# Performance work log

Measured on AMD Instinct MI355X. Metric: run time of the kernel, lower is better.

The kernel has to match this reference:

```python
import jax, jax.numpy as jnp
import numpy as np

B, T, C = 2, 2048, 1024
N_HEAD = 16
D_HEAD = C // N_HEAD


def setup_inputs() -> dict:
    key = jax.random.key(0)
    ks = jax.random.split(key, 5)
    x = jax.random.normal(ks[0], (B, T, C), dtype=jnp.float32)
    W_attn = jax.random.normal(ks[1], (C, 3 * C), dtype=jnp.float32) * (1.0 / np.sqrt(C))
    b_attn = jax.random.normal(ks[2], (3 * C,), dtype=jnp.float32) * 0.02
    W_proj = jax.random.normal(ks[3], (C, C), dtype=jnp.float32) * (1.0 / np.sqrt(C))
    b_proj = jax.random.normal(ks[4], (C,), dtype=jnp.float32) * 0.02
    return {"x": x, "W_attn": W_attn, "b_attn": b_attn, "W_proj": W_proj, "b_proj": b_proj}


def reference(x, W_attn, b_attn, W_proj, b_proj):
    b, t, c = x.shape
    nh, dh = N_HEAD, c // N_HEAD
    # qkv projection: (B, T, 3C) -> (B, T, 3, nh, dh) -> (B, nh, 3, T, dh)
    a = (x @ W_attn + b_attn).reshape(b, t, 3, nh, dh).transpose(0, 3, 2, 1, 4)
    Q, K, V = a[:, :, 0], a[:, :, 1], a[:, :, 2]  # each (B, nh, T, dh)
    # naive full attention: no causal mask, no pre-softmax scaling (as in source)
    scores = jnp.einsum('bhqd,bhkd->bhqk', Q, K)  # (B, nh, T, T) -- 512 MB
    att = jax.nn.softmax(scores, axis=-1)
    y = jnp.einsum('bhqk,bhkd->bhqd', att, V) / jnp.sqrt(jnp.asarray(dh, x.dtype))
    y = y.transpose(0, 2, 1, 3).reshape(b, t, c)  # (B, T, C)
    return y @ W_proj + b_proj
```

## Files before the change

### kernel.cpp

```cpp
#include <hip/hip_runtime.h>

typedef _Float16 f16;
typedef f16  f16x8 __attribute__((ext_vector_type(8)));
typedef f16  f16x4 __attribute__((ext_vector_type(4)));
typedef float f32x4 __attribute__((ext_vector_type(4)));
typedef int  i32x4 __attribute__((ext_vector_type(4)));

#define MFMA16(a,b,c) __builtin_amdgcn_mfma_f32_16x16x32_f16((a),(b),(c),0,0,0)
#define EXP2(x) __builtin_amdgcn_exp2f(x)
#define LOG2E 1.44269504089f

static constexpr int Tq   = 2048;
static constexpr int Cdim = 1024;

__device__ static inline void gload_lds16(const f16* gsrc, f16* ldst)
{
    __builtin_amdgcn_global_load_lds(
        (const __attribute__((address_space(1))) void*)gsrc,
        (__attribute__((address_space(3))) void*)ldst, 16, 0, 0);
}

__global__ __launch_bounds__(256) void k_cvt_x(const float* __restrict__ x, f16* __restrict__ xh)
{
    int i = blockIdx.x * 256 + threadIdx.x;
    f32x4 v = ((const f32x4*)x)[i];
    f16x4 o; o[0] = (f16)v[0]; o[1] = (f16)v[1]; o[2] = (f16)v[2]; o[3] = (f16)v[3];
    ((f16x4*)xh)[i] = o;
}

__global__ __launch_bounds__(256) void k_trans(const float* __restrict__ W, f16* __restrict__ WT,
                                               int K, int N)
{
    __shared__ float t[64][65];
    int n0 = blockIdx.x * 64, k0 = blockIdx.y * 64;
    int tid = threadIdx.x;
    int lr = tid >> 6, lc = tid & 63;
    #pragma unroll 4
    for (int i = 0; i < 16; i++) {
        int kl = lr * 16 + i;
        t[kl][lc] = W[(size_t)(k0 + kl) * N + n0 + lc];
    }
    __syncthreads();
    #pragma unroll 4
    for (int i = 0; i < 16; i++) {
        int nl = lr * 16 + i;
        WT[(size_t)(n0 + nl) * K + k0 + lc] = (f16)t[lc][nl];
    }
}

template<int EPI>
__global__ __launch_bounds__(256) void k_gemm(
    const f16* __restrict__ A, const f16* __restrict__ BT, const float* __restrict__ bias,
    float* __restrict__ Cf, f16* __restrict__ Qc, f16* __restrict__ Kc, f16* __restrict__ Vt,
    int N, int K)
{
    __shared__ __align__(16) f16 As[128][64];
    __shared__ __align__(16) f16 Bs[128][64];
    const int tid = threadIdx.x;
    const int lane = tid & 63, wv = tid >> 6;
    const int l16 = lane & 15, lhi = lane >> 4;
    const int wr = wv >> 1, wc = wv & 1;
    const int bm = blockIdx.y * 128, bn = blockIdx.x * 128;

    const int srow = lane >> 3;
    const int sch  = (lane & 7) ^ (srow & 7);

    f32x4 acc[4][4] = {};

    for (int kt = 0; kt < K; kt += 64) {
        #pragma unroll
        for (int i = 0; i < 4; i++) {
            int blk = wv * 4 + i;
            int row = blk * 8 + srow;
            gload_lds16(A  + (size_t)(bm + row) * K + kt + sch * 8, &As[blk * 8][0]);
            gload_lds16(BT + (size_t)(bn + row) * K + kt + sch * 8, &Bs[blk * 8][0]);
        }
        __syncthreads();
        #pragma unroll
        for (int kk = 0; kk < 2; kk++) {
            f16x8 af[4], bfr[4];
            #pragma unroll
            for (int i = 0; i < 4; i++) {
                int ra = wr * 64 + i * 16 + l16;
                af[i]  = *(const f16x8*)&As[ra][((kk * 4 + lhi) ^ (ra & 7)) * 8];
                int rb = wc * 64 + i * 16 + l16;
                bfr[i] = *(const f16x8*)&Bs[rb][((kk * 4 + lhi) ^ (rb & 7)) * 8];
            }
            #pragma unroll
            for (int i = 0; i < 4; i++)
                #pragma unroll
                for (int j = 0; j < 4; j++)
                    acc[i][j] = MFMA16(af[i], bfr[j], acc[i][j]);
        }
        __syncthreads();
    }

    #pragma unroll
    for (int i = 0; i < 4; i++) {
        int row0 = bm + wr * 64 + i * 16 + lhi * 4;
        #pragma unroll
        for (int j = 0; j < 4; j++) {
            int col = bn + wc * 64 + j * 16 + l16;
            float bv = bias[col];
            if (EPI == 0) {
                #pragma unroll
                for (int r = 0; r < 4; r++)
                    Cf[(size_t)(row0 + r) * N + col] = acc[i][j][r] + bv;
            } else {
                int b_ = row0 >> 11;
                int t0 = row0 & 2047;
                int s  = col >> 10;
                int h  = (col >> 6) & 15;
                int d  = col & 63;
                int bh = b_ * 16 + h;
                if (s < 2) {
                    f16* dst = (s == 0 ? Qc : Kc);
                    #pragma unroll
                    for (int r = 0; r < 4; r++)
                        dst[((size_t)bh * Tq + t0 + r) * 64 + d] = (f16)(acc[i][j][r] + bv);
                } else {
                    f16x4 p;
                    #pragma unroll
                    for (int r = 0; r < 4; r++) p[r] = (f16)(acc[i][j][r] + bv);
                    *(f16x4*)&Vt[((size_t)bh * 64 + d) * Tq + t0] = p;
                }
            }
        }
    }
}

__global__ __launch_bounds__(256) void k_attn(
    const f16* __restrict__ Qc, const f16* __restrict__ Kc, const f16* __restrict__ Vt,
    f16* __restrict__ Yc)
{
    __shared__ __align__(16) f16 Ks[2][64][64];
    __shared__ __align__(16) f16 Vs[2][64][64];

    const int tid = threadIdx.x;
    const int lane = tid & 63, wv = tid >> 6;
    const int l16 = lane & 15, lhi = lane >> 4;
    const int bh = blockIdx.y;
    const int q0 = blockIdx.x * 64;

    const f16* Qh = Qc + (size_t)bh * Tq * 64;
    const f16* Kh = Kc + (size_t)bh * Tq * 64;
    const f16* Vh = Vt + (size_t)bh * 64 * Tq;

    const int row0 = tid >> 3, ch0 = tid & 7;
    const int rp0  = (((row0 >> 2) & 1) << 4) | (((row0 >> 4) & 1) << 3)
                   | (((row0 >> 3) & 1) << 2) | (row0 & 3);
    const int pchK = ch0 ^ (rp0 & 7);
    const int pchV = ch0 ^ (row0 & 7);

    f16x8 qf[2];
    {
        int qrow = q0 + wv * 16 + l16;
        #pragma unroll
        for (int kk = 0; kk < 2; kk++)
            qf[kk] = *(const f16x8*)(Qh + (size_t)qrow * 64 + kk * 32 + lhi * 8);
    }

    f32x4 o[4] = {};
    float m2 = -3e38f, l = 0.0f;

    f16x8 kr0, kr1, vr0, vr1;
    kr0 = *(const f16x8*)(Kh + (size_t)row0 * 64 + ch0 * 8);
    kr1 = *(const f16x8*)(Kh + (size_t)(row0 + 32) * 64 + ch0 * 8);
    vr0 = *(const f16x8*)(Vh + (size_t)row0 * Tq + ch0 * 8);
    vr1 = *(const f16x8*)(Vh + (size_t)(row0 + 32) * Tq + ch0 * 8);
    *(f16x8*)&Ks[0][rp0][pchK * 8]       = kr0;
    *(f16x8*)&Ks[0][rp0 + 32][pchK * 8]  = kr1;
    *(f16x8*)&Vs[0][row0][pchV * 8]      = vr0;
    *(f16x8*)&Vs[0][row0 + 32][pchV * 8] = vr1;
    __syncthreads();

    int cur = 0;
    for (int t = 0; t < 32; t++) {
        if (t < 31) {
            int kt2 = (t + 1) * 64;
            kr0 = *(const f16x8*)(Kh + (size_t)(kt2 + row0) * 64 + ch0 * 8);
            kr1 = *(const f16x8*)(Kh + (size_t)(kt2 + row0 + 32) * 64 + ch0 * 8);
            vr0 = *(const f16x8*)(Vh + (size_t)row0 * Tq + kt2 + ch0 * 8);
            vr1 = *(const f16x8*)(Vh + (size_t)(row0 + 32) * Tq + kt2 + ch0 * 8);
        }

        const f16 (* __restrict__ Kb)[64] = Ks[cur];
        const f16 (* __restrict__ Vb)[64] = Vs[cur];

        f32x4 s[4];
        __builtin_amdgcn_s_setprio(1);
        #pragma unroll
        for (int ck = 0; ck < 4; ck++) {
            f32x4 acc = {};
            #pragma unroll
            for (int kk = 0; kk < 2; kk++) {
                f16x8 kf = *(const f16x8*)&Kb[ck * 16 + l16][((kk * 4 + lhi) ^ (l16 & 7)) * 8];
                acc = MFMA16(kf, qf[kk], acc);
            }
            s[ck] = acc;
        }
        __builtin_amdgcn_s_setprio(0);

        float tm = fmaxf(
            fmaxf(fmaxf(fmaxf(s[0][0], s[0][1]), fmaxf(s[0][2], s[0][3])),
                  fmaxf(fmaxf(s[1][0], s[1][1]), fmaxf(s[1][2], s[1][3]))),
            fmaxf(fmaxf(fmaxf(s[2][0], s[2][1]), fmaxf(s[2][2], s[2][3])),
                  fmaxf(fmaxf(s[3][0], s[3][1]), fmaxf(s[3][2], s[3][3]))));
        tm = fmaxf(tm, __shfl_xor(tm, 16));
        tm = fmaxf(tm, __shfl_xor(tm, 32));

        if (!__all(tm - m2 <= 8.0f)) {
            float mn = fmaxf(m2, tm);
            float sc = EXP2((m2 - mn) * LOG2E);
            m2 = mn; l *= sc;
            #pragma unroll
            for (int ct = 0; ct < 4; ct++)
                #pragma unroll
                for (int r = 0; r < 4; r++)
                    o[ct][r] *= sc;
        }

        float nm2 = -m2 * LOG2E;
        f32x4 p[4];
        #pragma unroll
        for (int ck = 0; ck < 4; ck++)
            #pragma unroll
            for (int r = 0; r < 4; r++)
                p[ck][r] = EXP2(fmaf(s[ck][r], LOG2E, nm2));

        float su = ((p[0][0] + p[0][1]) + (p[0][2] + p[0][3]))
                 + ((p[1][0] + p[1][1]) + (p[1][2] + p[1][3]))
                 + ((p[2][0] + p[2][1]) + (p[2][2] + p[2][3]))
                 + ((p[3][0] + p[3][1]) + (p[3][2] + p[3][3]));
        su += __shfl_xor(su, 16);
        su += __shfl_xor(su, 32);
        l += su;

        __builtin_amdgcn_s_setprio(1);
        #pragma unroll
        for (int kk2 = 0; kk2 < 2; kk2++) {
            i32x4 w;
            w[0] = __builtin_bit_cast(int, __builtin_amdgcn_cvt_pkrtz(p[2*kk2][0],   p[2*kk2][1]));
            w[1] = __builtin_bit_cast(int, __builtin_amdgcn_cvt_pkrtz(p[2*kk2][2],   p[2*kk2][3]));
            w[2] = __builtin_bit_cast(int, __builtin_amdgcn_cvt_pkrtz(p[2*kk2+1][0], p[2*kk2+1][1]));
            w[3] = __builtin_bit_cast(int, __builtin_amdgcn_cvt_pkrtz(p[2*kk2+1][2], p[2*kk2+1][3]));
            f16x8 pb = __builtin_bit_cast(f16x8, w);
            #pragma unroll
            for (int ct = 0; ct < 4; ct++) {
                f16x8 vf = *(const f16x8*)&Vb[ct * 16 + l16][((kk2 * 4 + lhi) ^ (l16 & 7)) * 8];
                o[ct] = MFMA16(vf, pb, o[ct]);
            }
        }
        __builtin_amdgcn_s_setprio(0);

        if (t < 31) {
            int nxt = cur ^ 1;
            *(f16x8*)&Ks[nxt][rp0][pchK * 8]       = kr0;
            *(f16x8*)&Ks[nxt][rp0 + 32][pchK * 8]  = kr1;
            *(f16x8*)&Vs[nxt][row0][pchV * 8]      = vr0;
            *(f16x8*)&Vs[nxt][row0 + 32][pchV * 8] = vr1;
            __syncthreads();
            cur = nxt;
        }
    }

    const int b_ = bh >> 4, h_ = bh & 15;
    const int q  = q0 + wv * 16 + l16;
    const float inv = 1.0f / (l * 8.0f);
    size_t rb = (size_t)(b_ * Tq + q) * Cdim + h_ * 64;
    #pragma unroll
    for (int ct = 0; ct < 4; ct++) {
        f16x4 y;
        #pragma unroll
        for (int r = 0; r < 4; r++) y[r] = (f16)(o[ct][r] * inv);
        *(f16x4*)&Yc[rb + ct * 16 + lhi * 4] = y;
    }
}

extern "C" void kernel_launch(void* const* d_in, const int* in_sizes, int n_in,
                              void* d_out, int out_size, void* d_ws, size_t ws_size,
                              hipStream_t stream)
{
    (void)in_sizes; (void)n_in; (void)out_size; (void)ws_size;
    const float* x  = (const float*)d_in[0];
    const float* Wa = (const float*)d_in[1];
    const float* ba = (const float*)d_in[2];
    const float* Wp = (const float*)d_in[3];
    const float* bp = (const float*)d_in[4];
    float* out = (float*)d_out;

    char* ws = (char*)d_ws;
    f16* Xh  = (f16*)(ws);
    f16* WaT = (f16*)(ws + (8u  << 20));
    f16* WpT = (f16*)(ws + (14u << 20));
    f16* Qc  = (f16*)(ws + (16u << 20));
    f16* Kc  = (f16*)(ws + (24u << 20));
    f16* Vt  = (f16*)(ws + (32u << 20));
    f16* Yc  = (f16*)(ws + (40u << 20));

    k_cvt_x<<<4096, 256, 0, stream>>>(x, Xh);
    k_trans<<<dim3(48, 16), 256, 0, stream>>>(Wa, WaT, 1024, 3072);
    k_trans<<<dim3(16, 16), 256, 0, stream>>>(Wp, WpT, 1024, 1024);
    k_gemm<1><<<dim3(24, 32), 256, 0, stream>>>(Xh, WaT, ba, nullptr, Qc, Kc, Vt, 3072, 1024);
    k_attn<<<dim3(32, 32), 256, 0, stream>>>(Qc, Kc, Vt, Yc);
    k_gemm<0><<<dim3(8, 32), 256, 0, stream>>>(Yc, WpT, bp, out, nullptr, nullptr, nullptr, 1024, 1024);
}
```

Measured before the change: 214.0 us.

## Process two 16-row query groups per wave in attention to reuse K/V tiles

Each wave in the attention kernel now handles 32 query rows (two 16-row groups) instead of 16, so each block covers 128 queries and the grid halves to 16x32. Every K and V fragment read from LDS feeds two MFMAs, which halves LDS and global K/V traffic per query and the number of tile syncs. The cost is higher register pressure from doubled accumulators and score tiles. The grid also drops to 512 blocks, which lowers parallelism across the 256 CUs.

```diff
diff --git a/kernel.cpp b/kernel.cpp
--- a/kernel.cpp
+++ b/kernel.cpp
@@ -140,7 +140,7 @@
     const int lane = tid & 63, wv = tid >> 6;
     const int l16 = lane & 15, lhi = lane >> 4;
     const int bh = blockIdx.y;
-    const int q0 = blockIdx.x * 64;
+    const int q0 = blockIdx.x * 128;
 
     const f16* Qh = Qc + (size_t)bh * Tq * 64;
     const f16* Kh = Kc + (size_t)bh * Tq * 64;
@@ -152,16 +152,17 @@
     const int pchK = ch0 ^ (rp0 & 7);
     const int pchV = ch0 ^ (row0 & 7);
 
-    f16x8 qf[2];
-    {
-        int qrow = q0 + wv * 16 + l16;
+    f16x8 qf[2][2];
+    #pragma unroll
+    for (int qg = 0; qg < 2; qg++) {
+        int qrow = q0 + wv * 32 + qg * 16 + l16;
         #pragma unroll
         for (int kk = 0; kk < 2; kk++)
-            qf[kk] = *(const f16x8*)(Qh + (size_t)qrow * 64 + kk * 32 + lhi * 8);
-    }
-
-    f32x4 o[4] = {};
-    float m2 = -3e38f, l = 0.0f;
+            qf[qg][kk] = *(const f16x8*)(Qh + (size_t)qrow * 64 + kk * 32 + lhi * 8);
+    }
+
+    f32x4 o[2][4] = {};
+    float m2[2] = {-3e38f, -3e38f}, l[2] = {0.0f, 0.0f};
 
     f16x8 kr0, kr1, vr0, vr1;
     kr0 = *(const f16x8*)(Kh + (size_t)row0 * 64 + ch0 * 8);
@@ -187,68 +188,81 @@
         const f16 (* __restrict__ Kb)[64] = Ks[cur];
         const f16 (* __restrict__ Vb)[64] = Vs[cur];
 
-        f32x4 s[4];
+        f32x4 s[2][4] = {};
         __builtin_amdgcn_s_setprio(1);
         #pragma unroll
         for (int ck = 0; ck < 4; ck++) {
-            f32x4 acc = {};
             #pragma unroll
             for (int kk = 0; kk < 2; kk++) {
                 f16x8 kf = *(const f16x8*)&Kb[ck * 16 + l16][((kk * 4 + lhi) ^ (l16 & 7)) * 8];
-                acc = MFMA16(kf, qf[kk], acc);
-            }
-            s[ck] = acc;
+                s[0][ck] = MFMA16(kf, qf[0][kk], s[0][ck]);
+                s[1][ck] = MFMA16(kf, qf[1][kk], s[1][ck]);
+            }
         }
         __builtin_amdgcn_s_setprio(0);
 
-        float tm = fmaxf(
-            fmaxf(fmaxf(fmaxf(s[0][0], s[0][1]), fmaxf(s[0][2], s[0][3])),
-                  fmaxf(fmaxf(s[1][0], s[1][1]), fmaxf(s[1][2], s[1][3]))),
-            fmaxf(fmaxf(fmaxf(s[2][0], s[2][1]), fmaxf(s[2][2], s[2][3])),
-                  fmaxf(fmaxf(s[3][0], s[3][1]), fmaxf(s[3][2], s[3][3]))));
-        tm = fmaxf(tm, __shfl_xor(tm, 16));
-        tm = fmaxf(tm, __shfl_xor(tm, 32));
-
-        if (!__all(tm - m2 <= 8.0f)) {
-            float mn = fmaxf(m2, tm);
-            float sc = EXP2((m2 - mn) * LOG2E);
-            m2 = mn; l *= sc;
-            #pragma unroll
-            for (int ct = 0; ct < 4; ct++)
+        float tm[2];
+        #pragma unroll
+        for (int qg = 0; qg < 2; qg++) {
+            float v = fmaxf(
+                fmaxf(fmaxf(fmaxf(s[qg][0][0], s[qg][0][1]), fmaxf(s[qg][0][2], s[qg][0][3])),
+                      fmaxf(fmaxf(s[qg][1][0], s[qg][1][1]), fmaxf(s[qg][1][2], s[qg][1][3]))),
+                fmaxf(fmaxf(fmaxf(s[qg][2][0], s[qg][2][1]), fmaxf(s[qg][2][2], s[qg][2][3])),
+                      fmaxf(fmaxf(s[qg][3][0], s[qg][3][1]), fmaxf(s[qg][3][2], s[qg][3][3]))));
+            v = fmaxf(v, __shfl_xor(v, 16));
+            v = fmaxf(v, __shfl_xor(v, 32));
+            tm[qg] = v;
+        }
+
+        if (!__all((tm[0] - m2[0] <= 8.0f) && (tm[1] - m2[1] <= 8.0f))) {
+            #pragma unroll
+            for (int qg = 0; qg < 2; qg++) {
+                float mn = fmaxf(m2[qg], tm[qg]);
+                float sc = EXP2((m2[qg] - mn) * LOG2E);
+                m2[qg] = mn; l[qg] *= sc;
+                #pragma unroll
+                for (int ct = 0; ct < 4; ct++)
+                    #pragma unroll
+                    for (int r = 0; r < 4; r++)
+                        o[qg][ct][r] *= sc;
+            }
+        }
+
+        #pragma unroll
+        for (int qg = 0; qg < 2; qg++) {
+            float nm2 = -m2[qg] * LOG2E;
+            #pragma unroll
+            for (int ck = 0; ck < 4; ck++)
                 #pragma unroll
                 for (int r = 0; r < 4; r++)
-                    o[ct][r] *= sc;
-        }
-
-        float nm2 = -m2 * LOG2E;
-        f32x4 p[4];
-        #pragma unroll
-        for (int ck = 0; ck < 4; ck++)
-            #pragma unroll
-            for (int r = 0; r < 4; r++)
-                p[ck][r] = EXP2(fmaf(s[ck][r], LOG2E, nm2));
-
-        float su = ((p[0][0] + p[0][1]) + (p[0][2] + p[0][3]))
-                 + ((p[1][0] + p[1][1]) + (p[1][2] + p[1][3]))
-                 + ((p[2][0] + p[2][1]) + (p[2][2] + p[2][3]))
-                 + ((p[3][0] + p[3][1]) + (p[3][2] + p[3][3]));
-        su += __shfl_xor(su, 16);
-        su += __shfl_xor(su, 32);
-        l += su;
+                    s[qg][ck][r] = EXP2(fmaf(s[qg][ck][r], LOG2E, nm2));
+            float su = ((s[qg][0][0] + s[qg][0][1]) + (s[qg][0][2] + s[qg][0][3]))
+                     + ((s[qg][1][0] + s[qg][1][1]) + (s[qg][1][2] + s[qg][1][3]))
+                     + ((s[qg][2][0] + s[qg][2][1]) + (s[qg][2][2] + s[qg][2][3]))
+                     + ((s[qg][3][0] + s[qg][3][1]) + (s[qg][3][2] + s[qg][3][3]));
+            su += __shfl_xor(su, 16);
+            su += __shfl_xor(su, 32);
+            l[qg] += su;
+        }
 
         __builtin_amdgcn_s_setprio(1);
         #pragma unroll
         for (int kk2 = 0; kk2 < 2; kk2++) {
-            i32x4 w;
-            w[0] = __builtin_bit_cast(int, __builtin_amdgcn_cvt_pkrtz(p[2*kk2][0],   p[2*kk2][1]));
-            w[1] = __builtin_bit_cast(int, __builtin_amdgcn_cvt_pkrtz(p[2*kk2][2],   p[2*kk2][3]));
-            w[2] = __builtin_bit_cast(int, __builtin_amdgcn_cvt_pkrtz(p[2*kk2+1][0], p[2*kk2+1][1]));
-            w[3] = __builtin_bit_cast(int, __builtin_amdgcn_cvt_pkrtz(p[2*kk2+1][2], p[2*kk2+1][3]));
-            f16x8 pb = __builtin_bit_cast(f16x8, w);
+            f16x8 pb[2];
+            #pragma unroll
+            for (int qg = 0; qg < 2; qg++) {
+                i32x4 w;
+                w[0] = __builtin_bit_cast(int, __builtin_amdgcn_cvt_pkrtz(s[qg][2*kk2][0],   s[qg][2*kk2][1]));
+                w[1] = __builtin_bit_cast(int, __builtin_amdgcn_cvt_pkrtz(s[qg][2*kk2][2],   s[qg][2*kk2][3]));
+                w[2] = __builtin_bit_cast(int, __builtin_amdgcn_cvt_pkrtz(s[qg][2*kk2+1][0], s[qg][2*kk2+1][1]));
+                w[3] = __builtin_bit_cast(int, __builtin_amdgcn_cvt_pkrtz(s[qg][2*kk2+1][2], s[qg][2*kk2+1][3]));
+                pb[qg] = __builtin_bit_cast(f16x8, w);
+            }
             #pragma unroll
             for (int ct = 0; ct < 4; ct++) {
                 f16x8 vf = *(const f16x8*)&Vb[ct * 16 + l16][((kk2 * 4 + lhi) ^ (l16 & 7)) * 8];
-                o[ct] = MFMA16(vf, pb, o[ct]);
+                o[0][ct] = MFMA16(vf, pb[0], o[0][ct]);
+                o[1][ct] = MFMA16(vf, pb[1], o[1][ct]);
             }
         }
         __builtin_amdgcn_s_setprio(0);
@@ -265,15 +279,18 @@
     }
 
     const int b_ = bh >> 4, h_ = bh & 15;
-    const int q  = q0 + wv * 16 + l16;
-    const float inv = 1.0f / (l * 8.0f);
-    size_t rb = (size_t)(b_ * Tq + q) * Cdim + h_ * 64;
     #pragma unroll
-    for (int ct = 0; ct < 4; ct++) {
-        f16x4 y;
-        #pragma unroll
-        for (int r = 0; r < 4; r++) y[r] = (f16)(o[ct][r] * inv);
-        *(f16x4*)&Yc[rb + ct * 16 + lhi * 4] = y;
+    for (int qg = 0; qg < 2; qg++) {
+        const int q = q0 + wv * 32 + qg * 16 + l16;
+        const float inv = 1.0f / (l[qg] * 8.0f);
+        size_t rb = (size_t)(b_ * Tq + q) * Cdim + h_ * 64;
+        #pragma unroll
+        for (int ct = 0; ct < 4; ct++) {
+            f16x4 y;
+            #pragma unroll
+            for (int r = 0; r < 4; r++) y[r] = (f16)(o[qg][ct][r] * inv);
+            *(f16x4*)&Yc[rb + ct * 16 + lhi * 4] = y;
+        }
     }
 }
 
@@ -302,6 +319,6 @@
     k_trans<<<dim3(48, 16), 256, 0, stream>>>(Wa, WaT, 1024, 3072);
     k_trans<<<dim3(16, 16), 256, 0, stream>>>(Wp, WpT, 1024, 1024);
     k_gemm<1><<<dim3(24, 32), 256, 0, stream>>>(Xh, WaT, ba, nullptr, Qc, Kc, Vt, 3072, 1024);
-    k_attn<<<dim3(32, 32), 256, 0, stream>>>(Qc, Kc, Vt, Yc);
+    k_attn<<<dim3(16, 32), 256, 0, stream>>>(Qc, Kc, Vt, Yc);
     k_gemm<0><<<dim3(8, 32), 256, 0, stream>>>(Yc, WpT, bp, out, nullptr, nullptr, nullptr, 1024, 1024);
 }
```

Measured after the change: 208.6 us. -2.5%, faster.
